# Performance work log

Measured on AMD Instinct MI355X. Metric: run time of the kernel, lower is better.

The kernel has to match this reference:

```python
import jax, jax.numpy as jnp
import numpy as np


def setup_inputs() -> dict:
    key = jax.random.key(0)
    x = jax.random.normal(key, (16, 256, 256, 64), dtype=jnp.float32)
    return {"x": x, "n_components": 32}


def reference(x, n_components):
    B = x.shape[0]
    C = x.shape[-1]
    # flatten spatial dims: [B, N, C]
    flat = x.reshape(B, -1, C)
    N = flat.shape[1]
    mean = jnp.mean(flat, axis=1, keepdims=True)
    centered = flat - mean
    # per-batch covariance [B, C, C]
    cov = jnp.einsum('bnc,bnd->bcd', centered, centered) / jnp.float32(N - 1)
    eigenvalues, eigenvectors = jnp.linalg.eigh(cov)
    # sort eigenvectors by descending eigenvalue, keep top n_components columns
    idx = jnp.argsort(-eigenvalues, axis=-1)  # [B, C]
    top = jnp.take_along_axis(eigenvectors, idx[:, None, :], axis=-1)[:, :, :n_components]
    # project: [B, N, k]
    projected = jnp.einsum('bnc,bck->bnk', centered, top)
    return projected.reshape(x.shape[:-1] + (n_components,))
```

## Files before the change

kernel.cpp:

```cpp
#include <hip/hip_runtime.h>
#include <hip/hip_bf16.h>


__device__ __forceinline__ double fsign(double a, double b){ return (b >= 0.0) ? fabs(a) : -fabs(a); }
__device__ __forceinline__ double slapy2(double x, double y){ return sqrt(x*x + y*y); }

__device__ __forceinline__ void slartg(double f, double g, double& cs, double& sn, double& r){
  if (g == 0.0){ cs = 1.0; sn = 0.0; r = f; }
  else if (f == 0.0){ cs = 0.0; sn = fsign(1.0, g); r = fabs(g); }
  else {
    double d = sqrt(f*f + g*g);
    cs = fabs(f)/d;
    r  = fsign(d, f);
    sn = g/r;
  }
}

__device__ __forceinline__ void slaev2(double a, double b, double c,
                                       double& rt1, double& rt2, double& cs1, double& sn1){
  double sm = a + c, df = a - c, adf = fabs(df), tb = b + b, ab = fabs(tb);
  double acmx, acmn, rt, cs, ct, acs, tn; int sgn1, sgn2;
  if (fabs(a) > fabs(c)) { acmx = a; acmn = c; } else { acmx = c; acmn = a; }
  if (adf > ab)      rt = adf*sqrt(1.0 + (ab/adf)*(ab/adf));
  else if (adf < ab) rt = ab*sqrt(1.0 + (adf/ab)*(adf/ab));
  else               rt = ab*sqrt(2.0);
  if (sm < 0.0){ rt1 = 0.5*(sm - rt); sgn1 = -1; rt2 = (acmx/rt1)*acmn - (b/rt1)*b; }
  else if (sm > 0.0){ rt1 = 0.5*(sm + rt); sgn1 = 1; rt2 = (acmx/rt1)*acmn - (b/rt1)*b; }
  else { rt1 = 0.5*rt; rt2 = -0.5*rt; sgn1 = 1; }
  if (df >= 0.0){ cs = df + rt; sgn2 = 1; } else { cs = df - rt; sgn2 = -1; }
  acs = fabs(cs);
  if (acs > ab){ ct = -tb/cs; sn1 = 1.0/sqrt(1.0 + ct*ct); cs1 = ct*sn1; }
  else {
    if (ab == 0.0){ cs1 = 1.0; sn1 = 0.0; }
    else { tn = -cs/tb; cs1 = 1.0/sqrt(1.0 + tn*tn); sn1 = tn*cs1; }
  }
  if (sgn1 == sgn2){ tn = cs1; cs1 = -sn1; sn1 = tn; }
}

__device__ __forceinline__ double wave_sum(double v){
  #pragma unroll
  for (int off = 32; off > 0; off >>= 1) v += __shfl_xor(v, off);
  return v;
}

template<int LDZ>
__device__ void steqr16(double* dd, double* ee, double* Zt, int tid,
                        double* wc, double* wsn)
{
#define DQ(i) dd[(i)-1]
#define EQ(i) ee[(i)-1]
#define ZT(r,c) Zt[(r)*LDZ+(c)]
  const int n = 16;
  const double eps = 5.9604644775390625e-8;
  const double eps2 = eps*eps;
  const double safmin = 1.1754943508222875e-38;
  const int nmaxit = n*30;
  int jtot = 0, l1 = 1, nm1 = n-1;
  int l, lsv, lend, lendsv, m, i;
  double p, g, r, s, c, f, b2, rt1, rt2, anorm, tst;

L10:
  if (l1 > n) goto L160;
  if (l1 > 1) EQ(l1-1) = 0.0;
  if (l1 <= nm1){
    for (m = l1; m <= nm1; ++m){
      tst = fabs(EQ(m));
      if (tst == 0.0) goto L30;
      if (tst <= (sqrt(fabs(DQ(m)))*sqrt(fabs(DQ(m+1))))*eps){ EQ(m) = 0.0; goto L30; }
    }
  }
  m = n;
L30:
  l = l1; lsv = l; lend = m; lendsv = lend; l1 = m+1;
  if (lend == l) goto L10;
  anorm = 0.0;
  for (i = l; i <= lend; ++i) anorm = fmax(anorm, fabs(DQ(i)));
  for (i = l; i <  lend; ++i) anorm = fmax(anorm, fabs(EQ(i)));
  if (anorm == 0.0) goto L10;
  if (fabs(DQ(lend)) < fabs(DQ(l))){ lend = lsv; l = lendsv; }
  if (lend > l){
L40:
    if (l != lend){
      for (m = l; m <= lend-1; ++m){
        tst = fabs(EQ(m)); tst = tst*tst;
        if (tst <= (eps2*fabs(DQ(m)))*fabs(DQ(m+1)) + safmin) goto L60;
      }
    }
    m = lend;
L60:
    if (m < lend) EQ(m) = 0.0;
    p = DQ(l);
    if (m == l) goto L80;
    if (m == l+1){
      slaev2(DQ(l), EQ(l), DQ(l+1), rt1, rt2, c, s);
      if (tid < 16){
        double t = ZT(tid, l);
        ZT(tid, l)   = c*t - s*ZT(tid, l-1);
        ZT(tid, l-1) = s*t + c*ZT(tid, l-1);
      }
      DQ(l) = rt1; DQ(l+1) = rt2; EQ(l) = 0.0;
      l += 2;
      if (l <= lend) goto L40;
      goto L140;
    }
    if (jtot == nmaxit) goto L140;
    jtot++;
    g = (DQ(l+1)-p)/(2.0*EQ(l));
    r = slapy2(g, 1.0);
    g = DQ(m) - p + (EQ(l)/(g + fsign(r, g)));
    s = 1.0; c = 1.0; p = 0.0;
    for (i = m-1; i >= l; --i){
      f = s*EQ(i); b2 = c*EQ(i);
      slartg(g, f, c, s, r);
      if (i != m-1) EQ(i+1) = r;
      g = DQ(i+1) - p;
      r = (DQ(i)-g)*s + 2.0*c*b2;
      p = s*r;
      DQ(i+1) = g + p;
      g = c*r - b2;
      wc[i] = c; wsn[i] = -s;
    }
    for (int i2 = m-1; i2 >= l; --i2){
      double cc = wc[i2], ssv = wsn[i2];
      if (tid < 16){
        double t = ZT(tid, i2);
        ZT(tid, i2)   = cc*t - ssv*ZT(tid, i2-1);
        ZT(tid, i2-1) = ssv*t + cc*ZT(tid, i2-1);
      }
    }
    DQ(l) = DQ(l) - p;
    EQ(l) = g;
    goto L40;
L80:
    DQ(l) = p;
    l++;
    if (l <= lend) goto L40;
    goto L140;
  } else {
L90:
    if (l != lend){
      for (m = l; m >= lend+1; --m){
        tst = fabs(EQ(m-1)); tst = tst*tst;
        if (tst <= (eps2*fabs(DQ(m)))*fabs(DQ(m-1)) + safmin) goto L110;
      }
    }
    m = lend;
L110:
    if (m > lend) EQ(m-1) = 0.0;
    p = DQ(l);
    if (m == l) goto L130;
    if (m == l-1){
      slaev2(DQ(l-1), EQ(l-1), DQ(l), rt1, rt2, c, s);
      if (tid < 16){
        double t = ZT(tid, l-1);
        ZT(tid, l-1) = c*t - s*ZT(tid, l-2);
        ZT(tid, l-2) = s*t + c*ZT(tid, l-2);
      }
      DQ(l-1) = rt1; DQ(l) = rt2; EQ(l-1) = 0.0;
      l -= 2;
      if (l >= lend) goto L90;
      goto L140;
    }
    if (jtot == nmaxit) goto L140;
    jtot++;
    g = (DQ(l-1)-p)/(2.0*EQ(l-1));
    r = slapy2(g, 1.0);
    g = DQ(m) - p + (EQ(l-1)/(g + fsign(r, g)));
    s = 1.0; c = 1.0; p = 0.0;
    for (i = m; i <= l-1; ++i){
      f = s*EQ(i); b2 = c*EQ(i);
      slartg(g, f, c, s, r);
      if (i != m) EQ(i-1) = r;
      g = DQ(i) - p;
      r = (DQ(i+1)-g)*s + 2.0*c*b2;
      p = s*r;
      DQ(i) = g + p;
      g = c*r - b2;
      wc[i] = c; wsn[i] = s;
    }
    for (int i2 = m; i2 <= l-1; ++i2){
      double cc = wc[i2], ssv = wsn[i2];
      if (tid < 16){
        double t = ZT(tid, i2);
        ZT(tid, i2)   = cc*t - ssv*ZT(tid, i2-1);
        ZT(tid, i2-1) = ssv*t + cc*ZT(tid, i2-1);
      }
    }
    DQ(l) = DQ(l) - p;
    EQ(l-1) = g;
    goto L90;
L130:
    DQ(l) = p;
    l--;
    if (l >= lend) goto L90;
    goto L140;
  }
L140:
  if (jtot < nmaxit) goto L10;
L160:
  for (int ii = 2; ii <= n; ++ii){
    int i3 = ii-1, k2 = i3;
    p = DQ(i3);
    for (int j = ii; j <= n; ++j) if (DQ(j) < p){ k2 = j; p = DQ(j); }
    if (k2 != i3){
      DQ(k2) = DQ(i3); DQ(i3) = p;
      if (tid < 16){
        double t = ZT(tid, i3-1);
        ZT(tid, i3-1) = ZT(tid, k2-1);
        ZT(tid, k2-1) = t;
      }
    }
  }
#undef DQ
#undef EQ
#undef ZT
}

template<int N1, int LD>
__device__ void merge_dc(double* Z, double* dloc, double rho_in, int tid,
                         double* zz, double* dl, double* ww, double* mu, double* wt,
                         int* idxm, int* sv, int* tl, int* fperm)
{
  const int NM = 2*N1;
  const int Q  = NM/4;
  const double eps32 = 5.9604644775390625e-8;
  const int j4 = tid >> 2, part = tid & 3;
  __shared__ int s_kn[2];

  if (tid < N1)       zz[tid] = Z[(N1-1)*LD + tid];
  else if (tid < NM)  zz[tid] = Z[N1*LD + tid];
  __syncthreads();
  if (rho_in < 0.0 && tid >= N1 && tid < NM) zz[tid] = -zz[tid];
  __syncthreads();
  if (tid < NM) zz[tid] *= 0.70710678118654752440;
  __syncthreads();
  double rho = fabs(2.0*rho_in);

  {
    int i1 = 0, i2 = 0, t = 0;
    while (i1 < N1 && i2 < N1){
      if (dloc[i1] <= dloc[N1+i2]) idxm[t++] = i1++;
      else                         idxm[t++] = N1 + (i2++);
    }
    while (i1 < N1) idxm[t++] = i1++;
    while (i2 < N1) idxm[t++] = N1 + (i2++);
  }
  double dmax = 0.0, zmax = 0.0;
  for (int i = 0; i < NM; ++i){ dmax = fmax(dmax, fabs(dloc[i])); zmax = fmax(zmax, fabs(zz[i])); }
  double tol = 8.0*eps32*fmax(dmax, zmax);

  if (rho*zmax <= tol){
    double colr[Q]; double dnj = 0.0;
    if (j4 < NM){
      int s0 = idxm[j4];
      dnj = dloc[s0];
      #pragma unroll
      for (int rr = 0; rr < Q; ++rr) colr[rr] = Z[(part+4*rr)*LD + s0];
    }
    __syncthreads();
    if (j4 < NM){
      #pragma unroll
      for (int rr = 0; rr < Q; ++rr) Z[(part+4*rr)*LD + j4] = colr[rr];
      if (part == 0) dloc[j4] = dnj;
    }
    __syncthreads();
    return;
  }

  int K, nd;
  if (tid < 64){
    K = 0; nd = 0;
    int have = 0, pj = 0;
    for (int t = 0; t < NM; ++t){
      int nj = idxm[t];
      if (rho*fabs(zz[nj]) <= tol){
        for (int q = nd; q > 0; --q) tl[q] = tl[q-1];
        tl[0] = nj; nd++;
        continue;
      }
      if (!have){ pj = nj; have = 1; continue; }
      {
        double sZ = zz[pj], cZ = zz[nj];
        double tau2 = slapy2(cZ, sZ);
        double tgap = dloc[nj] - dloc[pj];
        cZ /= tau2; sZ = -sZ/tau2;
        if (fabs(tgap*cZ*sZ) <= tol){
          zz[nj] = tau2; zz[pj] = 0.0;
          if (tid < NM){
            double xq = Z[tid*LD + pj], yq = Z[tid*LD + nj];
            Z[tid*LD + pj] = cZ*xq + sZ*yq;
            Z[tid*LD + nj] = cZ*yq - sZ*xq;
          }
          double t2 = dloc[pj]*cZ*cZ + dloc[nj]*sZ*sZ;
          double t3 = dloc[pj]*sZ*sZ + dloc[nj]*cZ*cZ;
          dloc[nj] = t3; dloc[pj] = t2;
          for (int q = nd; q > 0; --q) tl[q] = tl[q-1];
          tl[0] = pj; nd++;
          { int q = 0;
            while (q+1 < nd && dloc[tl[q]] < dloc[tl[q+1]]){
              int tt = tl[q]; tl[q] = tl[q+1]; tl[q+1] = tt; q++;
            } }
          pj = nj;
        } else {
          sv[K] = pj; dl[K] = dloc[pj]; ww[K] = zz[pj]; K++;
          pj = nj;
        }
      }
    }
    sv[K] = pj; dl[K] = dloc[pj]; ww[K] = zz[pj]; K++;
    if (tid == 0){ s_kn[0] = K; s_kn[1] = nd; }
  }
  __syncthreads();
  K = s_kn[0]; nd = s_kn[1];

  if (j4 < K){
    double dj = dl[j4];
    double dlr[Q], wr[Q];
    double zs2p = 0.0;
    #pragma unroll
    for (int t = 0; t < Q; ++t){
      int i = part + 4*t;
      if (i < K){ double wv = ww[i]; dlr[t] = dl[i]; wr[t] = rho*wv*wv; zs2p += wv*wv; }
      else      { dlr[t] = 1.0e300; wr[t] = 0.0; }
    }
    zs2p += __shfl_xor(zs2p, 1); zs2p += __shfl_xor(zs2p, 2);
    double lo = 0.0, hi = (j4 < K-1) ? (dl[j4+1]-dj) : rho*zs2p;
    for (int it = 0; it < 24; ++it){
      double mid = 0.5*(lo+hi);
      if (mid == lo || mid == hi) break;
      double fvp = 0.0;
      #pragma unroll
      for (int t = 0; t < Q; ++t) fvp += wr[t]/((dlr[t]-dj) - mid);
      fvp += __shfl_xor(fvp, 1); fvp += __shfl_xor(fvp, 2);
      double fv = 1.0 + fvp;
      if (fv < 0.0) lo = mid; else hi = mid;
    }
    double muv = 0.5*(lo+hi);
    for (int it = 0; it < 14; ++it){
      double fvp = 0.0, fpp = 0.0;
      #pragma unroll
      for (int t = 0; t < Q; ++t){
        double den = (dlr[t]-dj) - muv;
        double inv = 1.0/den;
        double tq = wr[t]*inv;
        fvp += tq; fpp += tq*inv;
      }
      fvp += __shfl_xor(fvp, 1); fvp += __shfl_xor(fvp, 2);
      fpp += __shfl_xor(fpp, 1); fpp += __shfl_xor(fpp, 2);
      double fv = 1.0 + fvp;
      if (fv == 0.0) break;
      if (fv < 0.0) lo = muv; else hi = muv;
      double mn = muv - fv/fpp;
      if (!(mn > lo && mn < hi)) mn = 0.5*(lo+hi);
      if (mn == muv) break;
      muv = mn;
    }
    if (part == 0) mu[j4] = muv;
  }
  __syncthreads();

  if (j4 < K){
    double dj = dl[j4];
    double pp = 1.0;
    for (int i2 = part; i2 < K; i2 += 4){
      if (i2 == j4) continue;
      double dij = dj - dl[i2];
      pp *= (dij - mu[i2])/dij;
    }
    pp *= __shfl_xor(pp, 1); pp *= __shfl_xor(pp, 2);
    double prod = -mu[j4]*pp;
    if (part == 0) wt[j4] = fsign(sqrt(fmax(-prod, 0.0)), ww[j4]);
  }
  __syncthreads();

  {
    int a = 0, q = nd-1, t = 0;
    while (a < K && q >= 0){
      if (dl[a]+mu[a] <= dloc[tl[q]]) { fperm[t++] = a; a++; }
      else { fperm[t++] = K+q; q--; }
    }
    while (a < K)  { fperm[t++] = a; a++; }
    while (q >= 0) { fperm[t++] = K+q; q--; }
  }
  __syncthreads();

  double colr[Q]; double dnj = 0.0;
  if (j4 < NM){
    int src = fperm[j4];
    if (src < K){
      double muj = mu[src];
      double ds  = dl[src];
      double nrmp = 0.0;
      for (int i = part; i < K; i += 4){
        double del = (dl[i]-ds) - muj;
        double qv = wt[i]/del;
        nrmp += qv*qv;
      }
      nrmp += __shfl_xor(nrmp, 1); nrmp += __shfl_xor(nrmp, 2);
      double invn = 1.0/sqrt(nrmp);
      #pragma unroll
      for (int rr = 0; rr < Q; ++rr) colr[rr] = 0.0;
      for (int i = 0; i < K; ++i){
        double del = (dl[i]-ds) - muj;
        double sval = (wt[i]/del)*invn;
        int cq = sv[i];
        #pragma unroll
        for (int rr = 0; rr < Q; ++rr) colr[rr] += Z[(part+4*rr)*LD + cq]*sval;
      }
      dnj = ds + muj;
    } else {
      int tq2 = tl[src-K];
      #pragma unroll
      for (int rr = 0; rr < Q; ++rr) colr[rr] = Z[(part+4*rr)*LD + tq2];
      dnj = dloc[tq2];
    }
  }
  __syncthreads();
  if (j4 < NM){
    #pragma unroll
    for (int rr = 0; rr < Q; ++rr) Z[(part+4*rr)*LD + j4] = colr[rr];
    if (part == 0) dloc[j4] = dnj;
  }
  __syncthreads();
}

__global__ __launch_bounds__(256) void cov_kernel(const float* __restrict__ x,
                                                  double* __restrict__ gram,
                                                  double* __restrict__ chsum)
{
  __shared__ __align__(16) float tile[32][64];
  const int b   = blockIdx.x >> 5;
  const int ch  = blockIdx.x & 31;
  const int tid = threadIdx.x;
  const int ti = tid >> 4, tj = tid & 15;
  const int lrow = tid >> 4, lf4 = tid & 15;
  const int cch = tid & 63, crr = tid >> 6;
  float acc[4][4];
  #pragma unroll
  for (int a = 0; a < 4; ++a)
    #pragma unroll
    for (int c = 0; c < 4; ++c) acc[a][c] = 0.f;
  float csum = 0.f;
  const float* xb = x + ((size_t)b*65536 + (size_t)ch*2048)*64;
  float4 v0 = *(const float4*)(xb + (size_t)(lrow     )*64 + lf4*4);
  float4 v1 = *(const float4*)(xb + (size_t)(lrow + 16)*64 + lf4*4);
  for (int r0 = 0; r0 < 2048; r0 += 32){
    __syncthreads();
    *(float4*)&tile[lrow][lf4*4]      = v0;
    *(float4*)&tile[16 + lrow][lf4*4] = v1;
    __syncthreads();
    if (r0 + 32 < 2048){
      v0 = *(const float4*)(xb + (size_t)(r0 + 32 + lrow)*64 + lf4*4);
      v1 = *(const float4*)(xb + (size_t)(r0 + 48 + lrow)*64 + lf4*4);
    }
    #pragma unroll
    for (int rr = 0; rr < 32; ++rr){
      float4 xi = *(const float4*)&tile[rr][4*ti];
      float4 xj = *(const float4*)&tile[rr][4*tj];
      acc[0][0] += xi.x*xj.x; acc[0][1] += xi.x*xj.y; acc[0][2] += xi.x*xj.z; acc[0][3] += xi.x*xj.w;
      acc[1][0] += xi.y*xj.x; acc[1][1] += xi.y*xj.y; acc[1][2] += xi.y*xj.z; acc[1][3] += xi.y*xj.w;
      acc[2][0] += xi.z*xj.x; acc[2][1] += xi.z*xj.y; acc[2][2] += xi.z*xj.z; acc[2][3] += xi.z*xj.w;
      acc[3][0] += xi.w*xj.x; acc[3][1] += xi.w*xj.y; acc[3][2] += xi.w*xj.z; acc[3][3] += xi.w*xj.w;
    }
    #pragma unroll
    for (int rr2 = 0; rr2 < 8; ++rr2) csum += tile[crr + rr2*4][cch];
  }
  double* gb = gram + (size_t)b*4096;
  #pragma unroll
  for (int a = 0; a < 4; ++a)
    #pragma unroll
    for (int c = 0; c < 4; ++c)
      atomicAdd(&gb[(4*ti+a)*64 + (4*tj+c)], (double)acc[a][c]);
  atomicAdd(&chsum[b*64 + cch], (double)csum);
}

__global__ __launch_bounds__(64) void tridiag_kernel(const double* __restrict__ gram,
                                                     const double* __restrict__ chsum,
                                                     double* __restrict__ dG,
                                                     double* __restrict__ eG,
                                                     double* __restrict__ tauG,
                                                     double* __restrict__ VlG,
                                                     float* __restrict__ meanG)
{
  __shared__ double As[64*65];
  __shared__ double vv_[64], wv_[64], mu_s[64], es_s[64], tau_s[64];
  const int b = blockIdx.x;
  const int tid = threadIdx.x;
  const double* gb = gram + (size_t)b*4096;

  double mval = chsum[b*64+tid]*(1.0/65536.0);
  meanG[b*64+tid] = (float)mval;
  mu_s[tid] = mval;
  __syncthreads();
  for (int idx = tid; idx < 4096; idx += 64){
    int i = idx >> 6, j = idx & 63;
    As[i*65+j] = (gb[idx] - 65536.0*mu_s[i]*mu_s[j])*(1.0/65535.0);
  }
  __syncthreads();

  for (int i = 0; i < 63; ++i){
    double alpha = As[(i+1)*65+i];
    double xv0 = (tid >= i+2) ? As[tid*65+i] : 0.0;
    double xn2 = wave_sum(xv0*xv0);
    if (xn2 == 0.0){
      es_s[i] = alpha; tau_s[i] = 0.0;
      VlG[((size_t)b*63 + i)*64 + tid] = 0.0;
      __syncthreads();
      continue;
    }
    double xnorm = sqrt(xn2);
    double betav = -fsign(slapy2(alpha, xnorm), alpha);
    double taui  = (betav-alpha)/betav;
    double invs  = 1.0/(alpha-betav);
    double vval = (tid == i+1) ? 1.0 : ((tid >= i+2) ? xv0*invs : 0.0);
    vv_[tid] = vval;
    VlG[((size_t)b*63 + i)*64 + tid] = vval;
    __syncthreads();
    double x0 = 0.0, x1 = 0.0, x2 = 0.0, x3 = 0.0;
    #pragma unroll
    for (int c2 = 0; c2 < 64; c2 += 4){
      x0 += As[tid*65+c2+0]*vv_[c2+0];
      x1 += As[tid*65+c2+1]*vv_[c2+1];
      x2 += As[tid*65+c2+2]*vv_[c2+2];
      x3 += As[tid*65+c2+3]*vv_[c2+3];
    }
    double xvr = ((x0+x1)+(x2+x3))*taui;
    double dot = wave_sum((tid >= i+1) ? xvr*vval : 0.0);
    double alf = -0.5*taui*dot;
    wv_[tid] = (tid >= i+1) ? (xvr + alf*vval) : 0.0;
    __syncthreads();
    {
      double vr = vval, wr = wv_[tid];
      #pragma unroll
      for (int c2 = 0; c2 < 64; ++c2)
        As[tid*65+c2] -= vr*wv_[c2] + wr*vv_[c2];
    }
    es_s[i] = betav; tau_s[i] = taui;
    __syncthreads();
  }
  dG[b*64+tid]   = As[tid*65+tid];
  eG[b*64+tid]   = (tid < 63) ? es_s[tid]  : 0.0;
  tauG[b*64+tid] = (tid < 63) ? tau_s[tid] : 0.0;
}

__global__ __launch_bounds__(64) void steqr_kernel(double* __restrict__ dG,
                                                   const double* __restrict__ eG,
                                                   double* __restrict__ Zg)
{
  __shared__ double Zt[16*17];
  __shared__ double dd[16], ee[16], wc[20], wsn[20];
  const int b = blockIdx.x >> 2, s = blockIdx.x & 3;
  const int tid = threadIdx.x;

  {
    double dv = (tid < 16) ? dG[b*64 + 16*s + tid] : 0.0;
    if (tid == 0  && s > 0) dv -= fabs(eG[b*64 + 16*s - 1]);
    if (tid == 15 && s < 3) dv -= fabs(eG[b*64 + 16*s + 15]);
    if (tid < 16) dd[tid] = dv;
    if (tid < 15) ee[tid] = eG[b*64 + 16*s + tid];
    if (tid == 15) ee[15] = 0.0;
  }
  for (int idx = tid; idx < 16*17; idx += 64) Zt[idx] = 0.0;
  __syncthreads();
  if (tid < 16) Zt[tid*17+tid] = 1.0;
  __syncthreads();

  steqr16<17>(dd, ee, Zt, tid, wc, wsn);
  __syncthreads();

  for (int idx = tid; idx < 256; idx += 64){
    int r = idx >> 4, c = idx & 15;
    Zg[(size_t)b*4096 + s*256 + idx] = Zt[r*17+c];
  }
  if (tid < 16) dG[b*64 + 16*s + tid] = dd[tid];
}

__global__ __launch_bounds__(256) void merge16_kernel(double* __restrict__ Zg,
                                                      double* __restrict__ dG,
                                                      const double* __restrict__ eG)
{
  __shared__ double Z32[32*33];
  __shared__ double dloc[32];
  __shared__ double zz[32], dl[32], ww[32], mu[32], wt[32];
  __shared__ int idxm[32], sv[32], tl[32], fp[32];
  const int b = blockIdx.x >> 1, h = blockIdx.x & 1;
  const int tid = threadIdx.x;

  for (int idx = tid; idx < 32*33; idx += 256) Z32[idx] = 0.0;
  if (tid < 32) dloc[tid] = dG[b*64 + 32*h + tid];
  __syncthreads();
  {
    int idx = tid;
    int r = idx >> 4, c = idx & 15;
    Z32[r*33 + c]           = Zg[(size_t)b*4096 + (2*h)*256   + idx];
    Z32[(16+r)*33 + (16+c)] = Zg[(size_t)b*4096 + (2*h+1)*256 + idx];
  }
  __syncthreads();

  double rho_in = eG[b*64 + 32*h + 15];
  merge_dc<16,33>(Z32, dloc, rho_in, tid, zz, dl, ww, mu, wt, idxm, sv, tl, fp);

  for (int idx = tid; idx < 1024; idx += 256){
    int r = idx >> 5, c = idx & 31;
    Zg[(size_t)b*4096 + 2048 + h*1024 + idx] = Z32[r*33 + c];
  }
  if (tid < 32) dG[b*64 + 32*h + tid] = dloc[tid];
}

__global__ __launch_bounds__(256) void merge32_bt_kernel(const double* __restrict__ Zg,
                                                         double* __restrict__ dG,
                                                         const double* __restrict__ eG,
                                                         const double* __restrict__ tauG,
                                                         const double* __restrict__ VlG,
                                                         float* __restrict__ Vt)
{
  __shared__ double Z64[64*65];
  __shared__ double Vl_s[63*64];
  __shared__ double dloc[64], tau_l[64];
  __shared__ double zz[64], dl[64], ww[64], mu[64], wt[64];
  __shared__ int idxm[64], sv[64], tl[64], fp[64];
  const int b = blockIdx.x;
  const int tid = threadIdx.x;

  for (int idx = tid; idx < 64*65; idx += 256) Z64[idx] = 0.0;
  if (tid < 64){ dloc[tid] = dG[b*64 + tid]; tau_l[tid] = tauG[b*64 + tid]; }
  for (int idx = tid; idx < 63*64; idx += 256) Vl_s[idx] = VlG[(size_t)b*63*64 + idx];
  __syncthreads();
  for (int idx = tid; idx < 1024; idx += 256){
    int r = idx >> 5, c = idx & 31;
    Z64[r*65 + c]           = Zg[(size_t)b*4096 + 2048 + idx];
    Z64[(32+r)*65 + (32+c)] = Zg[(size_t)b*4096 + 3072 + idx];
  }
  __syncthreads();

  double rho_in = eG[b*64 + 31];
  merge_dc<32,65>(Z64, dloc, rho_in, tid, zz, dl, ww, mu, wt, idxm, sv, tl, fp);

  {
    const int jc = tid >> 2, part = tid & 3;
    double z[16];
    #pragma unroll
    for (int rr = 0; rr < 16; ++rr) z[rr] = Z64[(part + 4*rr)*65 + jc];
    for (int i = 62; i >= 0; --i){
      double taui = tau_l[i];
      if (taui == 0.0) continue;
      double vir[16];
      #pragma unroll
      for (int rr = 0; rr < 16; ++rr) vir[rr] = Vl_s[i*64 + part + 4*rr];
      double w0 = 0.0, w1 = 0.0;
      #pragma unroll
      for (int rr = 0; rr < 16; rr += 2){ w0 += vir[rr]*z[rr]; w1 += vir[rr+1]*z[rr+1]; }
      double w = w0 + w1;
      w += __shfl_xor(w, 1);
      w += __shfl_xor(w, 2);
      w *= taui;
      #pragma unroll
      for (int rr = 0; rr < 16; ++rr) z[rr] -= vir[rr]*w;
    }
    #pragma unroll
    for (int rr = 0; rr < 16; ++rr) Z64[(part + 4*rr)*65 + jc] = z[rr];
  }
  __syncthreads();

  for (int idx = tid; idx < 2048; idx += 256){
    int c2 = idx >> 5, k = idx & 31;
    Vt[(size_t)b*2048 + idx] = (float)Z64[c2*65 + (63-k)];
  }
}

__global__ __launch_bounds__(256) void proj_kernel(const float* __restrict__ x,
                                                   const float* __restrict__ Vt,
                                                   const float* __restrict__ meanf,
                                                   float* __restrict__ out)
{
  __shared__ __align__(16) float Vs[64][32];
  __shared__ float ms[64];
  const int b = blockIdx.x >> 8;
  const int rb = blockIdx.x & 255;
  const int tid = threadIdx.x;
  for (int idx = tid; idx < 2048; idx += 256) ((float*)Vs)[idx] = Vt[(size_t)b*2048 + idx];
  if (tid < 64) ms[tid] = meanf[b*64+tid];
  __syncthreads();
  const size_t row = (size_t)b*65536 + (size_t)rb*256 + tid;
  const float4* xr = (const float4*)(x + row*64);
  float acc[32];
  #pragma unroll
  for (int k = 0; k < 32; ++k) acc[k] = 0.f;
  #pragma unroll
  for (int c4 = 0; c4 < 16; ++c4){
    float4 xv = xr[c4];
    float t0 = xv.x - ms[4*c4+0];
    float t1 = xv.y - ms[4*c4+1];
    float t2 = xv.z - ms[4*c4+2];
    float t3 = xv.w - ms[4*c4+3];
    #pragma unroll
    for (int k4 = 0; k4 < 8; ++k4){
      const float4 a0 = *(const float4*)&Vs[4*c4+0][4*k4];
      const float4 a1 = *(const float4*)&Vs[4*c4+1][4*k4];
      const float4 a2 = *(const float4*)&Vs[4*c4+2][4*k4];
      const float4 a3 = *(const float4*)&Vs[4*c4+3][4*k4];
      acc[4*k4+0] += t0*a0.x + t1*a1.x + t2*a2.x + t3*a3.x;
      acc[4*k4+1] += t0*a0.y + t1*a1.y + t2*a2.y + t3*a3.y;
      acc[4*k4+2] += t0*a0.z + t1*a1.z + t2*a2.z + t3*a3.z;
      acc[4*k4+3] += t0*a0.w + t1*a1.w + t2*a2.w + t3*a3.w;
    }
  }
  float4* op = (float4*)(out + row*32);
  #pragma unroll
  for (int k4 = 0; k4 < 8; ++k4)
    op[k4] = make_float4(acc[4*k4], acc[4*k4+1], acc[4*k4+2], acc[4*k4+3]);
}

extern "C" void kernel_launch(void* const* d_in, const int* in_sizes, int n_in,
                              void* d_out, int out_size, void* d_ws, size_t ws_size,
                              hipStream_t stream)
{
  const float* x = (const float*)d_in[0];
  float* out = (float*)d_out;
  char* ws = (char*)d_ws;
  double* gram  = (double*)(ws);
  double* Zg    = (double*)(ws);
  double* chsum = (double*)(ws + 524288);
  double* dG    = (double*)(ws + 532480);
  double* eG    = (double*)(ws + 540672);
  double* tauG  = (double*)(ws + 548864);
  double* VlG   = (double*)(ws + 557056);
  float*  Vt    = (float*) (ws + 1073152);
  float*  mf    = (float*) (ws + 1204224);

  hipMemsetAsync(ws, 0, 532480, stream);
  cov_kernel     <<<dim3(512),  dim3(256), 0, stream>>>(x, gram, chsum);
  tridiag_kernel <<<dim3(16),   dim3(64),  0, stream>>>(gram, chsum, dG, eG, tauG, VlG, mf);
  steqr_kernel   <<<dim3(64),   dim3(64),  0, stream>>>(dG, eG, Zg);
  merge16_kernel <<<dim3(32),   dim3(256), 0, stream>>>(Zg, dG, eG);
  merge32_bt_kernel<<<dim3(16), dim3(256), 0, stream>>>(Zg, dG, eG, tauG, VlG, Vt);
  proj_kernel    <<<dim3(4096), dim3(256), 0, stream>>>(x, Vt, mf, out);
}
```

Before: 1.034 ms.

## Split tridiagonal reduction matvec and rank-2 update across four waves

The Householder tridiagonalization kernel now runs 256 threads per batch instead of 64. Each of the four waves handles a 16-column slice of the symmetric matvec and of the rank-2 update, and partial sums are combined through shared memory. This targets the serial latency of the 63-step reduction, which runs on only 16 blocks. In exchange it adds an extra barrier and a shared-memory reduction step per iteration.

```diff
diff --git a/kernel.cpp b/kernel.cpp
--- a/kernel.cpp
+++ b/kernel.cpp
@@ -474,25 +474,31 @@
   atomicAdd(&chsum[b*64 + cch], (double)csum);
 }
 
-__global__ __launch_bounds__(64) void tridiag_kernel(const double* __restrict__ gram,
-                                                     const double* __restrict__ chsum,
-                                                     double* __restrict__ dG,
-                                                     double* __restrict__ eG,
-                                                     double* __restrict__ tauG,
-                                                     double* __restrict__ VlG,
-                                                     float* __restrict__ meanG)
+__global__ __launch_bounds__(256) void tridiag_kernel(const double* __restrict__ gram,
+                                                      const double* __restrict__ chsum,
+                                                      double* __restrict__ dG,
+                                                      double* __restrict__ eG,
+                                                      double* __restrict__ tauG,
+                                                      double* __restrict__ VlG,
+                                                      float* __restrict__ meanG)
 {
   __shared__ double As[64*65];
   __shared__ double vv_[64], wv_[64], mu_s[64], es_s[64], tau_s[64];
+  __shared__ double part_s[4*64];
   const int b = blockIdx.x;
   const int tid = threadIdx.x;
+  const int row = tid & 63;
+  const int wpart = tid >> 6;
+  const int cbase = wpart * 16;
   const double* gb = gram + (size_t)b*4096;
 
-  double mval = chsum[b*64+tid]*(1.0/65536.0);
-  meanG[b*64+tid] = (float)mval;
-  mu_s[tid] = mval;
-  __syncthreads();
-  for (int idx = tid; idx < 4096; idx += 64){
+  double mval = chsum[b*64+row]*(1.0/65536.0);
+  if (tid < 64){
+    meanG[b*64+row] = (float)mval;
+    mu_s[row] = mval;
+  }
+  __syncthreads();
+  for (int idx = tid; idx < 4096; idx += 256){
     int i = idx >> 6, j = idx & 63;
     As[i*65+j] = (gb[idx] - 65536.0*mu_s[i]*mu_s[j])*(1.0/65535.0);
   }
@@ -500,11 +506,13 @@
 
   for (int i = 0; i < 63; ++i){
     double alpha = As[(i+1)*65+i];
-    double xv0 = (tid >= i+2) ? As[tid*65+i] : 0.0;
+    double xv0 = (row >= i+2) ? As[row*65+i] : 0.0;
     double xn2 = wave_sum(xv0*xv0);
     if (xn2 == 0.0){
-      es_s[i] = alpha; tau_s[i] = 0.0;
-      VlG[((size_t)b*63 + i)*64 + tid] = 0.0;
+      if (tid < 64){
+        es_s[i] = alpha; tau_s[i] = 0.0;
+        VlG[((size_t)b*63 + i)*64 + row] = 0.0;
+      }
       __syncthreads();
       continue;
     }
@@ -512,35 +520,47 @@
     double betav = -fsign(slapy2(alpha, xnorm), alpha);
     double taui  = (betav-alpha)/betav;
     double invs  = 1.0/(alpha-betav);
-    double vval = (tid == i+1) ? 1.0 : ((tid >= i+2) ? xv0*invs : 0.0);
-    vv_[tid] = vval;
-    VlG[((size_t)b*63 + i)*64 + tid] = vval;
-    __syncthreads();
-    double x0 = 0.0, x1 = 0.0, x2 = 0.0, x3 = 0.0;
-    #pragma unroll
-    for (int c2 = 0; c2 < 64; c2 += 4){
-      x0 += As[tid*65+c2+0]*vv_[c2+0];
-      x1 += As[tid*65+c2+1]*vv_[c2+1];
-      x2 += As[tid*65+c2+2]*vv_[c2+2];
-      x3 += As[tid*65+c2+3]*vv_[c2+3];
-    }
-    double xvr = ((x0+x1)+(x2+x3))*taui;
-    double dot = wave_sum((tid >= i+1) ? xvr*vval : 0.0);
-    double alf = -0.5*taui*dot;
-    wv_[tid] = (tid >= i+1) ? (xvr + alf*vval) : 0.0;
+    double vval = (row == i+1) ? 1.0 : ((row >= i+2) ? xv0*invs : 0.0);
+    if (tid < 64){
+      vv_[row] = vval;
+      VlG[((size_t)b*63 + i)*64 + row] = vval;
+    }
     __syncthreads();
     {
-      double vr = vval, wr = wv_[tid];
-      #pragma unroll
-      for (int c2 = 0; c2 < 64; ++c2)
-        As[tid*65+c2] -= vr*wv_[c2] + wr*vv_[c2];
-    }
-    es_s[i] = betav; tau_s[i] = taui;
+      double p0 = 0.0, p1 = 0.0, p2 = 0.0, p3 = 0.0;
+      #pragma unroll
+      for (int k = 0; k < 16; k += 4){
+        p0 += As[row*65+cbase+k+0]*vv_[cbase+k+0];
+        p1 += As[row*65+cbase+k+1]*vv_[cbase+k+1];
+        p2 += As[row*65+cbase+k+2]*vv_[cbase+k+2];
+        p3 += As[row*65+cbase+k+3]*vv_[cbase+k+3];
+      }
+      part_s[wpart*64 + row] = (p0+p1)+(p2+p3);
+    }
     __syncthreads();
-  }
-  dG[b*64+tid]   = As[tid*65+tid];
-  eG[b*64+tid]   = (tid < 63) ? es_s[tid]  : 0.0;
-  tauG[b*64+tid] = (tid < 63) ? tau_s[tid] : 0.0;
+    double xvr = (part_s[row] + part_s[64+row]) + (part_s[128+row] + part_s[192+row]);
+    xvr = (row >= i+1) ? xvr*taui : 0.0;
+    double dot = wave_sum((row >= i+1) ? xvr*vval : 0.0);
+    double alf = -0.5*taui*dot;
+    double wvv = (row >= i+1) ? (xvr + alf*vval) : 0.0;
+    if (tid < 64) wv_[row] = wvv;
+    __syncthreads();
+    {
+      double vr = vval, wr = wvv;
+      #pragma unroll
+      for (int k = 0; k < 16; ++k){
+        int c = cbase + k;
+        As[row*65+c] -= vr*wv_[c] + wr*vv_[c];
+      }
+    }
+    if (tid < 64){ es_s[i] = betav; tau_s[i] = taui; }
+    __syncthreads();
+  }
+  if (tid < 64){
+    dG[b*64+row]   = As[row*65+row];
+    eG[b*64+row]   = (row < 63) ? es_s[row]  : 0.0;
+    tauG[b*64+row] = (row < 63) ? tau_s[row] : 0.0;
+  }
 }
 
 __global__ __launch_bounds__(64) void steqr_kernel(double* __restrict__ dG,
@@ -730,7 +750,7 @@
 
   hipMemsetAsync(ws, 0, 532480, stream);
   cov_kernel     <<<dim3(512),  dim3(256), 0, stream>>>(x, gram, chsum);
-  tridiag_kernel <<<dim3(16),   dim3(64),  0, stream>>>(gram, chsum, dG, eG, tauG, VlG, mf);
+  tridiag_kernel <<<dim3(16),   dim3(256), 0, stream>>>(gram, chsum, dG, eG, tauG, VlG, mf);
   steqr_kernel   <<<dim3(64),   dim3(64),  0, stream>>>(dG, eG, Zg);
   merge16_kernel <<<dim3(32),   dim3(256), 0, stream>>>(Zg, dG, eG);
   merge32_bt_kernel<<<dim3(16), dim3(256), 0, stream>>>(Zg, dG, eG, tauG, VlG, Vt);
```

New measurement: 981.3 us. 1.05x faster.
